# Kernel tuning notes

Hardware: AMD Instinct MI355X
Metric: run time of the kernel (lower is better)

## Reference

```python
import jax, jax.numpy as jnp
import numpy as np
from jax import lax

VOCAB = 400000
EMB = 300
HIDDEN = 128
OUT = 3
SEQ = 4096


def setup_inputs() -> dict:
    key = jax.random.key(0)
    ks = jax.random.split(key, 8)
    X = jax.random.randint(ks[0], (SEQ,), 0, VOCAB)
    weights = jax.random.normal(ks[1], (VOCAB, EMB), dtype=jnp.float32) * 0.1
    # nn.RNN params (tanh nonlinearity), uniform(-1/sqrt(H), 1/sqrt(H)) like torch
    s = 1.0 / np.sqrt(HIDDEN)
    W_ih = jax.random.uniform(ks[2], (HIDDEN, EMB), minval=-s, maxval=s, dtype=jnp.float32)
    b_ih = jax.random.uniform(ks[3], (HIDDEN,), minval=-s, maxval=s, dtype=jnp.float32)
    W_hh = jax.random.uniform(ks[4], (HIDDEN, HIDDEN), minval=-s, maxval=s, dtype=jnp.float32)
    b_hh = jax.random.uniform(ks[5], (HIDDEN,), minval=-s, maxval=s, dtype=jnp.float32)
    W_fc = jax.random.uniform(ks[6], (OUT, HIDDEN), minval=-s, maxval=s, dtype=jnp.float32)
    b_fc = jax.random.uniform(ks[7], (OUT,), minval=-s, maxval=s, dtype=jnp.float32)
    return {"X": X, "weights": weights, "W_ih": W_ih, "b_ih": b_ih,
            "W_hh": W_hh, "b_hh": b_hh, "W_fc": W_fc, "b_fc": b_fc}


def reference(X, weights, W_ih, b_ih, W_hh, b_hh, W_fc, b_fc):
    # embedding lookup: [S, E]
    emb = weights[X]
    # precompute input projections for all timesteps in one GEMM: [S, H]
    xproj = emb @ W_ih.T + b_ih
    h0 = jnp.zeros((HIDDEN,), dtype=weights.dtype)

    def step(h, xp):
        h_new = jnp.tanh(xp + h @ W_hh.T + b_hh)
        return h_new, None

    hT, _ = lax.scan(step, h0, xproj)  # Elman recurrence; hT is last-step output
    logits = hT @ W_fc.T + b_fc        # [OUT]; equals fc(yt).squeeze()
    return jax.nn.log_softmax(logits)  # log-softmax over the class dim
```

## Files before the change

kernel.cpp:

```cpp
#include <hip/hip_runtime.h>
#include <hip/hip_bf16.h>

#define VOCAB  400000
#define EMB    300
#define HIDDEN 128
#define OUT    3
#define SEQ    4096
#define SPB    8

__global__ __launch_bounds__(128) void xproj_kernel(
    const int* __restrict__ X, const float* __restrict__ weights,
    const float* __restrict__ W_ih, const float* __restrict__ b_ih,
    float* __restrict__ xproj)
{
    __shared__ float emb[SPB][EMB];
    __shared__ int xs[SPB];
    const int tid = threadIdx.x;
    const int s0 = blockIdx.x * SPB;

    if (tid < SPB) xs[tid] = X[s0 + tid];
    __syncthreads();

    {
        const float4* w4 = (const float4*)weights;
        float4* e4 = (float4*)&emb[0][0];
        for (int i = tid; i < SPB * (EMB / 4); i += 128) {
            int s = i / (EMB / 4);
            int r = i - s * (EMB / 4);
            e4[i] = w4[(size_t)xs[s] * (EMB / 4) + r];
        }
    }
    __syncthreads();

    const float4* wrow = (const float4*)(W_ih + tid * EMB);
    float acc[SPB];
    #pragma unroll
    for (int s = 0; s < SPB; ++s) acc[s] = 0.f;

    #pragma unroll 5
    for (int r = 0; r < EMB / 4; ++r) {
        float4 w = wrow[r];
        #pragma unroll
        for (int s = 0; s < SPB; ++s) {
            float4 e = *(const float4*)&emb[s][4 * r];
            acc[s] += w.x * e.x;
            acc[s] += w.y * e.y;
            acc[s] += w.z * e.z;
            acc[s] += w.w * e.w;
        }
    }

    const float b = b_ih[tid];
    #pragma unroll
    for (int s = 0; s < SPB; ++s)
        xproj[(size_t)(s0 + s) * HIDDEN + tid] = acc[s] + b;
}

__device__ __forceinline__ float quad_reduce_add(float x) {
    int t = __builtin_amdgcn_update_dpp(0, __float_as_int(x), 0xB1, 0xF, 0xF, true);
    x += __int_as_float(t);
    t = __builtin_amdgcn_update_dpp(0, __float_as_int(x), 0x4E, 0xF, 0xF, true);
    x += __int_as_float(t);
    return x;
}

__global__ __launch_bounds__(512) void rnn_scan_kernel(
    const float* __restrict__ xproj, const float* __restrict__ W_hh,
    const float* __restrict__ b_hh, const float* __restrict__ W_fc,
    const float* __restrict__ b_fc, float* __restrict__ out)
{
    __shared__ float h_lds[2][HIDDEN];
    __shared__ float lg[OUT];

    const int tid = threadIdx.x;
    const int o   = tid >> 2;
    const int q   = tid & 3;

    float4 w[8];
    {
        const float4* wr = (const float4*)(W_hh + o * HIDDEN);
        #pragma unroll
        for (int rr = 0; rr < 8; ++rr) w[rr] = wr[4 * rr + q];
    }
    const float bh = b_hh[o];

    if (tid < HIDDEN) h_lds[0][tid] = 0.f;
    float xp0 = xproj[o];
    float xp1 = xproj[HIDDEN + o];
    __syncthreads();

    int cur = 0;
    for (int t = 0; t < SEQ; ++t) {
        const int tn = (t + 2 < SEQ) ? t + 2 : SEQ - 1;
        float xp2 = xproj[(size_t)tn * HIDDEN + o];

        const float4* hb = (const float4*)&h_lds[cur][0] + q;
        float a0 = 0.f, a1 = 0.f, a2 = 0.f, a3 = 0.f;
        #pragma unroll
        for (int rr = 0; rr < 8; ++rr) {
            float4 hv = hb[4 * rr];
            a0 += hv.x * w[rr].x;
            a1 += hv.y * w[rr].y;
            a2 += hv.z * w[rr].z;
            a3 += hv.w * w[rr].w;
        }
        float acc = (a0 + a1) + (a2 + a3);
        acc = quad_reduce_add(acc);

        float z = acc + xp0 + bh;
        z = fminf(fmaxf(z, -15.f), 15.f);
        float e = __expf(2.f * z);
        float hn = (e - 1.f) * __builtin_amdgcn_rcpf(e + 1.f);
        if (q == 0) h_lds[cur ^ 1][o] = hn;

        __syncthreads();
        cur ^= 1;
        xp0 = xp1;
        xp1 = xp2;
    }

    if (tid < OUT) {
        float a = b_fc[tid];
        const float* wf = W_fc + tid * HIDDEN;
        #pragma unroll 4
        for (int j = 0; j < HIDDEN; ++j) a += h_lds[cur][j] * wf[j];
        lg[tid] = a;
    }
    __syncthreads();
    if (tid == 0) {
        float m = fmaxf(lg[0], fmaxf(lg[1], lg[2]));
        float s = expf(lg[0] - m) + expf(lg[1] - m) + expf(lg[2] - m);
        float lse = m + logf(s);
        out[0] = lg[0] - lse;
        out[1] = lg[1] - lse;
        out[2] = lg[2] - lse;
    }
}

extern "C" void kernel_launch(void* const* d_in, const int* in_sizes, int n_in,
                              void* d_out, int out_size, void* d_ws, size_t ws_size,
                              hipStream_t stream) {
    const int*   X       = (const int*)d_in[0];
    const float* weights = (const float*)d_in[1];
    const float* W_ih    = (const float*)d_in[2];
    const float* b_ih    = (const float*)d_in[3];
    const float* W_hh    = (const float*)d_in[4];
    const float* b_hh    = (const float*)d_in[5];
    const float* W_fc    = (const float*)d_in[6];
    const float* b_fc    = (const float*)d_in[7];
    float* out   = (float*)d_out;
    float* xproj = (float*)d_ws;

    xproj_kernel<<<SEQ / SPB, 128, 0, stream>>>(X, weights, W_ih, b_ih, xproj);
    rnn_scan_kernel<<<1, 512, 0, stream>>>(xproj, W_hh, b_hh, W_fc, b_fc, out);
}
```

Before: 1.833 ms.

## Stage xproj chunks into double-buffered LDS instead of per-step global loads

New measurement: 1.964 ms. 1.07x slower.

```diff
diff --git a/kernel.cpp b/kernel.cpp
--- a/kernel.cpp
+++ b/kernel.cpp
@@ -7,6 +7,10 @@
 #define OUT    3
 #define SEQ    4096
 #define SPB    8
+#define CHUNK  64
+#define NCHUNK (SEQ / CHUNK)
+
+typedef float f32x4 __attribute__((ext_vector_type(4)));
 
 __global__ __launch_bounds__(128) void xproj_kernel(
     const int* __restrict__ X, const float* __restrict__ weights,
@@ -64,50 +68,68 @@
     return x;
 }
 
-__global__ __launch_bounds__(512) void rnn_scan_kernel(
+__global__ __launch_bounds__(512, 2) void rnn_scan_kernel(
     const float* __restrict__ xproj, const float* __restrict__ W_hh,
     const float* __restrict__ b_hh, const float* __restrict__ W_fc,
     const float* __restrict__ b_fc, float* __restrict__ out)
 {
     __shared__ float h_lds[2][HIDDEN];
+    __shared__ float xp_lds[2][CHUNK * HIDDEN];
     __shared__ float lg[OUT];
 
     const int tid = threadIdx.x;
     const int o   = tid >> 2;
     const int q   = tid & 3;
 
-    float4 w[8];
+    f32x4 w[8];
     {
-        const float4* wr = (const float4*)(W_hh + o * HIDDEN);
+        const f32x4* wr = (const f32x4*)(W_hh + o * HIDDEN);
         #pragma unroll
         for (int rr = 0; rr < 8; ++rr) w[rr] = wr[4 * rr + q];
+        #pragma unroll
+        for (int rr = 0; rr < 8; ++rr) asm volatile("" : "+v"(w[rr]));
     }
     const float bh = b_hh[o];
 
+    const f32x4* xp_g4 = (const f32x4*)xproj;
+    f32x4 stg[4];
+    #pragma unroll
+    for (int i = 0; i < 4; ++i) stg[i] = xp_g4[i * 512 + tid];
+
     if (tid < HIDDEN) h_lds[0][tid] = 0.f;
-    float xp0 = xproj[o];
-    float xp1 = xproj[HIDDEN + o];
-    __syncthreads();
 
     int cur = 0;
     for (int t = 0; t < SEQ; ++t) {
-        const int tn = (t + 2 < SEQ) ? t + 2 : SEQ - 1;
-        float xp2 = xproj[(size_t)tn * HIDDEN + o];
+        const int tc = t & (CHUNK - 1);
+        const int cb = (t >> 6) & 1;
+        if (tc == 0) {
+            const int c = t >> 6;
+            f32x4* dst = (f32x4*)&xp_lds[c & 1][0];
+            #pragma unroll
+            for (int i = 0; i < 4; ++i) dst[i * 512 + tid] = stg[i];
+            __syncthreads();
+            const int cn = (c + 1 < NCHUNK) ? c + 1 : NCHUNK - 1;
+            #pragma unroll
+            for (int i = 0; i < 4; ++i)
+                stg[i] = xp_g4[(size_t)cn * (CHUNK * HIDDEN / 4) + i * 512 + tid];
+        }
 
-        const float4* hb = (const float4*)&h_lds[cur][0] + q;
+        const float xp = xp_lds[cb][tc * HIDDEN + o];
+
+        const f32x4* hb = (const f32x4*)&h_lds[cur][0] + q;
         float a0 = 0.f, a1 = 0.f, a2 = 0.f, a3 = 0.f;
         #pragma unroll
         for (int rr = 0; rr < 8; ++rr) {
-            float4 hv = hb[4 * rr];
-            a0 += hv.x * w[rr].x;
-            a1 += hv.y * w[rr].y;
-            a2 += hv.z * w[rr].z;
-            a3 += hv.w * w[rr].w;
+            f32x4 hv = hb[4 * rr];
+            a0 += hv[0] * w[rr][0];
+            a1 += hv[1] * w[rr][1];
+            a2 += hv[2] * w[rr][2];
+            a3 += hv[3] * w[rr][3];
         }
         float acc = (a0 + a1) + (a2 + a3);
         acc = quad_reduce_add(acc);
 
-        float z = acc + xp0 + bh;
+        float z = acc + xp + bh;
         z = fminf(fmaxf(z, -15.f), 15.f);
         float e = __expf(2.f * z);
         float hn = (e - 1.f) * __builtin_amdgcn_rcpf(e + 1.f);
@@ -115,8 +137,6 @@
 
         __syncthreads();
         cur ^= 1;
-        xp0 = xp1;
-        xp1 = xp2;
     }
 
     if (tid < OUT) {
```
